# Optimization experiments

Hardware: AMD Instinct MI355X
Metric: run time of the kernel (lower is better)

The kernel has to match this reference:

```python
import jax, jax.numpy as jnp
import numpy as np

N_NODES = 50000
N_EDGES = 1600000
D_IN = 128
D_HID = 128
D_OUT = 128


def setup_inputs() -> dict:
    key = jax.random.key(0)
    k = jax.random.split(key, 6)
    feat = jax.random.normal(k[0], (N_NODES, D_IN), dtype=jnp.float32)
    W1 = jax.random.normal(k[1], (D_IN, D_HID), dtype=jnp.float32) * (1.0 / np.sqrt(D_IN))
    b1 = jnp.zeros((D_HID,), dtype=jnp.float32)
    W2 = jax.random.normal(k[2], (D_HID, D_OUT), dtype=jnp.float32) * (1.0 / np.sqrt(D_HID))
    b2 = jnp.zeros((D_OUT,), dtype=jnp.float32)
    src = jax.random.randint(k[3], (N_EDGES,), 0, N_NODES, dtype=jnp.int32)
    dst = jax.random.randint(k[4], (N_EDGES,), 0, N_NODES, dtype=jnp.int32)
    return {"feat": feat, "W1": W1, "b1": b1, "W2": W2, "b2": b2, "src": src, "dst": dst}


def _graph_conv(h, W, b, src, dst, norm_src, norm_dst, n_nodes):
    # DGL GraphConv, norm='both': h_src * out_deg^-1/2 -> sum over edges -> * in_deg^-1/2 -> W, +b
    h = h * norm_src[:, None]
    agg = jax.ops.segment_sum(h[src], dst, num_segments=n_nodes)
    agg = agg * norm_dst[:, None]
    return agg @ W + b


def reference(feat, W1, b1, W2, b2, src, dst):
    n = feat.shape[0]
    # dgl.add_self_loop: append (i, i) for every node
    loop = jnp.arange(n, dtype=src.dtype)
    src = jnp.concatenate([src, loop])
    dst = jnp.concatenate([dst, loop])
    ones = jnp.ones(src.shape[0], dtype=feat.dtype)
    out_deg = jax.ops.segment_sum(ones, src, num_segments=n)  # >= 1 due to self-loops
    in_deg = jax.ops.segment_sum(ones, dst, num_segments=n)
    norm_src = jax.lax.rsqrt(out_deg)
    norm_dst = jax.lax.rsqrt(in_deg)
    h = _graph_conv(feat, W1, b1, src, dst, norm_src, norm_dst, n)
    h = jax.nn.relu(h)
    h = _graph_conv(h, W2, b2, src, dst, norm_src, norm_dst, n)
    return h[None, :, :]  # unsqueeze(0) -> [1, N, out_features]
```

## Files before the change

### kernel.cpp

```cpp
#include <hip/hip_runtime.h>

#define D 128
#define RANGES 4
#define CHUNKS 64
#define BINS_MAX 12512

typedef unsigned short u16;


__device__ __forceinline__ u16 f2bf(float x) {
  unsigned u = __float_as_uint(x);
  u += 0x7fffu + ((u >> 16) & 1u);
  return (u16)(u >> 16);
}
#define BF_LO(u) __uint_as_float((u) << 16)
#define BF_HI(u) __uint_as_float((u) & 0xffff0000u)


__global__ __launch_bounds__(1024)
void hist_kernel(const int* __restrict__ keys, u16* __restrict__ part,
                 int E, int N, int binsR, int chunkE)
{
  __shared__ int hist[BINS_MAX];
  const int b = blockIdx.x;
  const int r = b & (RANGES - 1);
  const int k = b >> 2;
  const int lo = r * binsR;
  const int hi = min(N, lo + binsR);
  const int nb = hi - lo;
  for (int i = threadIdx.x; i < nb; i += 1024) hist[i] = 0;
  __syncthreads();
  const int e0 = k * chunkE;
  const int e1 = min(E, e0 + chunkE);
  for (int e = e0 + threadIdx.x; e < e1; e += 1024) {
    int v = keys[e];
    if (v >= lo && v < hi) atomicAdd(&hist[v - lo], 1);
  }
  __syncthreads();
  for (int i = threadIdx.x; i < nb; i += 1024)
    part[(size_t)k * N + lo + i] = (u16)hist[i];
}

__global__ void reduce_kernel(const u16* __restrict__ psrc, u16* __restrict__ pdst,
                              int* __restrict__ deg_in, float* __restrict__ nsrc,
                              float* __restrict__ ndst, int N)
{
  int bin = blockIdx.x * blockDim.x + threadIdx.x;
  if (bin >= N) return;
  int runs = 0, rund = 0;
  for (int k = 0; k < CHUNKS; ++k) {
    runs += psrc[(size_t)k * N + bin];
    int vd = pdst[(size_t)k * N + bin];
    pdst[(size_t)k * N + bin] = (u16)rund;
    rund += vd;
  }
  deg_in[bin] = rund;
  nsrc[bin] = rsqrtf((float)runs + 1.0f);
  ndst[bin] = rsqrtf((float)rund + 1.0f);
}


__global__ __launch_bounds__(1024)
void scan1_kernel(const int* __restrict__ din, int* __restrict__ roff,
                  int* __restrict__ bsum, int N)
{
  __shared__ int wsum[16];
  const int t = threadIdx.x, lane = t & 63, wid = t >> 6;
  const int i = blockIdx.x * 1024 + t;
  int v = (i < N) ? din[i] : 0;
  int x = v;
  #pragma unroll
  for (int off = 1; off < 64; off <<= 1) {
    int u = __shfl_up(x, off);
    if (lane >= off) x += u;
  }
  if (lane == 63) wsum[wid] = x;
  __syncthreads();
  if (wid == 0) {
    int y = (lane < 16) ? wsum[lane] : 0;
    int z = y;
    #pragma unroll
    for (int off = 1; off < 16; off <<= 1) {
      int u = __shfl_up(z, off);
      if (lane >= off) z += u;
    }
    if (lane < 16) wsum[lane] = z - y;
    if (lane == 15) bsum[blockIdx.x] = z;
  }
  __syncthreads();
  if (i < N) roff[i] = wsum[wid] + (x - v);
}

__global__ void scan2_kernel(int* __restrict__ bsum, int* __restrict__ roffN, int nb)
{
  const int t = threadIdx.x;
  int v = (t < nb) ? bsum[t] : 0;
  int x = v;
  #pragma unroll
  for (int off = 1; off < 64; off <<= 1) {
    int u = __shfl_up(x, off);
    if (t >= off) x += u;
  }
  if (t < nb) bsum[t] = x - v;
  if (t == 63) *roffN = x;
}

__global__ __launch_bounds__(1024)
void scan3_kernel(int* __restrict__ roff, const int* __restrict__ bsum, int N)
{
  const int i = blockIdx.x * 1024 + threadIdx.x;
  if (i < N) roff[i] += bsum[i >> 10];
}


__global__ __launch_bounds__(1024)
void scatter_kernel(const int* __restrict__ src, const int* __restrict__ dst,
                    const u16* __restrict__ pdst, const int* __restrict__ roff,
                    int* __restrict__ eout, int E, int N, int binsR, int chunkE)
{
  __shared__ int cur[BINS_MAX];
  const int b = blockIdx.x;
  const int r = b & (RANGES - 1);
  const int k = b >> 2;
  const int lo = r * binsR;
  const int hi = min(N, lo + binsR);
  const int nb = hi - lo;
  for (int i = threadIdx.x; i < nb; i += 1024)
    cur[i] = roff[lo + i] + (int)pdst[(size_t)k * N + lo + i];
  __syncthreads();
  const int e0 = k * chunkE;
  const int e1 = min(E, e0 + chunkE);
  for (int e = e0 + threadIdx.x; e < e1; e += 1024) {
    int d = dst[e];
    if (d >= lo && d < hi) eout[atomicAdd(&cur[d - lo], 1)] = src[e];
  }
}


__global__ __launch_bounds__(256)
void convert_kernel(const float* __restrict__ f, const float* __restrict__ nsrc,
                    unsigned* __restrict__ fb, int n4)
{
  const int i = blockIdx.x * blockDim.x + threadIdx.x;
  if (i < n4) {
    float s = nsrc[i >> 5];
    float4 v = ((const float4*)f)[i];
    uint2 o;
    o.x = (unsigned)f2bf(v.x * s) | ((unsigned)f2bf(v.y * s) << 16);
    o.y = (unsigned)f2bf(v.z * s) | ((unsigned)f2bf(v.w * s) << 16);
    ((uint2*)fb)[i] = o;
  }
}


__global__ __launch_bounds__(256)
void gather_bf_kernel(const unsigned* __restrict__ fb, const int* __restrict__ eidx,
                      const int* __restrict__ roff, const float* __restrict__ ndst,
                      float* __restrict__ out, int N)
{
  const int wid = threadIdx.x >> 6;
  const int lane = threadIdx.x & 63;
  const int node = blockIdx.x * 4 + wid;
  if (node >= N) return;
  const int h = lane >> 5;
  const int q = lane & 31;
  const uint2* fb2 = (const uint2*)fb;
  float4 acc = make_float4(0.f, 0.f, 0.f, 0.f);
  if (h == 0) {
    uint2 u = fb2[(size_t)node * 32 + q];
    acc.x = BF_LO(u.x); acc.y = BF_HI(u.x);
    acc.z = BF_LO(u.y); acc.w = BF_HI(u.y);
  }
  const int beg = roff[node], end = roff[node + 1];
  for (int e0 = beg; e0 < end; e0 += 64) {
    const int cnt = min(64, end - e0);
    int id = (lane < cnt) ? eidx[e0 + lane] : 0;
    int j = 0;
    for (; j + 16 <= cnt; j += 16) {
      int s0 = __shfl(id, j + 0 + h);
      int s1 = __shfl(id, j + 2 + h);
      int s2 = __shfl(id, j + 4 + h);
      int s3 = __shfl(id, j + 6 + h);
      int s4 = __shfl(id, j + 8 + h);
      int s5 = __shfl(id, j + 10 + h);
      int s6 = __shfl(id, j + 12 + h);
      int s7 = __shfl(id, j + 14 + h);
      uint2 u0 = fb2[(size_t)s0 * 32 + q];
      uint2 u1 = fb2[(size_t)s1 * 32 + q];
      uint2 u2 = fb2[(size_t)s2 * 32 + q];
      uint2 u3 = fb2[(size_t)s3 * 32 + q];
      uint2 u4 = fb2[(size_t)s4 * 32 + q];
      uint2 u5 = fb2[(size_t)s5 * 32 + q];
      uint2 u6 = fb2[(size_t)s6 * 32 + q];
      uint2 u7 = fb2[(size_t)s7 * 32 + q];
      acc.x += BF_LO(u0.x); acc.y += BF_HI(u0.x); acc.z += BF_LO(u0.y); acc.w += BF_HI(u0.y);
      acc.x += BF_LO(u1.x); acc.y += BF_HI(u1.x); acc.z += BF_LO(u1.y); acc.w += BF_HI(u1.y);
      acc.x += BF_LO(u2.x); acc.y += BF_HI(u2.x); acc.z += BF_LO(u2.y); acc.w += BF_HI(u2.y);
      acc.x += BF_LO(u3.x); acc.y += BF_HI(u3.x); acc.z += BF_LO(u3.y); acc.w += BF_HI(u3.y);
      acc.x += BF_LO(u4.x); acc.y += BF_HI(u4.x); acc.z += BF_LO(u4.y); acc.w += BF_HI(u4.y);
      acc.x += BF_LO(u5.x); acc.y += BF_HI(u5.x); acc.z += BF_LO(u5.y); acc.w += BF_HI(u5.y);
      acc.x += BF_LO(u6.x); acc.y += BF_HI(u6.x); acc.z += BF_LO(u6.y); acc.w += BF_HI(u6.y);
      acc.x += BF_LO(u7.x); acc.y += BF_HI(u7.x); acc.z += BF_LO(u7.y); acc.w += BF_HI(u7.y);
    }
    for (; j < cnt; j += 2) {
      int ej = j + h;
      int s = __shfl(id, ej & 63);
      if (ej < cnt) {
        uint2 u = fb2[(size_t)s * 32 + q];
        acc.x += BF_LO(u.x); acc.y += BF_HI(u.x);
        acc.z += BF_LO(u.y); acc.w += BF_HI(u.y);
      }
    }
  }
  acc.x += __shfl_xor(acc.x, 32);
  acc.y += __shfl_xor(acc.y, 32);
  acc.z += __shfl_xor(acc.z, 32);
  acc.w += __shfl_xor(acc.w, 32);
  if (h == 0) {
    float nd = ndst[node];
    acc.x *= nd; acc.y *= nd; acc.z *= nd; acc.w *= nd;
    *(float4*)(out + (size_t)node * D + q * 4) = acc;
  }
}


template<bool RELU_SCALE, bool BF_OUT>
__global__ __launch_bounds__(256)
void gemm128(const float* __restrict__ A, const float* __restrict__ W,
             const float* __restrict__ bias, const float* __restrict__ nsrc,
             void* __restrict__ Cv, int N)
{
  __shared__ float As[64][36];
  __shared__ float Bs[32][128];
  const int t = threadIdx.x;
  const int tx = t & 15;
  const int ty = t >> 4;
  const int r0 = blockIdx.x * 64;
  float acc[4][8];
  #pragma unroll
  for (int j = 0; j < 4; ++j)
    #pragma unroll
    for (int cc = 0; cc < 8; ++cc) acc[j][cc] = 0.f;

  for (int kc = 0; kc < D; kc += 32) {
    __syncthreads();
    #pragma unroll
    for (int m = 0; m < 2; ++m) {
      int q = t * 2 + m;
      int row = q >> 3;
      int fc = q & 7;
      int gr = r0 + row; if (gr > N - 1) gr = N - 1;
      float4 v = *(const float4*)(A + (size_t)gr * D + kc + fc * 4);
      *(float4*)(&As[row][fc * 4]) = v;
    }
    #pragma unroll
    for (int m = 0; m < 4; ++m) {
      int q = t + 256 * m;
      int kk = q >> 5;
      int fc = q & 31;
      float4 v = *(const float4*)(W + (size_t)(kc + kk) * D + fc * 4);
      *(float4*)(&Bs[kk][fc * 4]) = v;
    }
    __syncthreads();
    #pragma unroll
    for (int k = 0; k < 32; ++k) {
      float a0 = As[ty * 4 + 0][k];
      float a1 = As[ty * 4 + 1][k];
      float a2 = As[ty * 4 + 2][k];
      float a3 = As[ty * 4 + 3][k];
      float4 bv0 = *(const float4*)(&Bs[k][tx * 4]);
      float4 bv1 = *(const float4*)(&Bs[k][64 + tx * 4]);
      float bb[8] = {bv0.x, bv0.y, bv0.z, bv0.w, bv1.x, bv1.y, bv1.z, bv1.w};
      #pragma unroll
      for (int cc = 0; cc < 8; ++cc) {
        acc[0][cc] += a0 * bb[cc];
        acc[1][cc] += a1 * bb[cc];
        acc[2][cc] += a2 * bb[cc];
        acc[3][cc] += a3 * bb[cc];
      }
    }
  }

  float4 bb0 = *(const float4*)(bias + tx * 4);
  float4 bb1 = *(const float4*)(bias + 64 + tx * 4);
  float bb[8] = {bb0.x, bb0.y, bb0.z, bb0.w, bb1.x, bb1.y, bb1.z, bb1.w};
  #pragma unroll
  for (int j = 0; j < 4; ++j) {
    int gr = r0 + ty * 4 + j;
    if (gr < N) {
      float s = RELU_SCALE ? nsrc[gr] : 1.0f;
      float o[8];
      #pragma unroll
      for (int cc = 0; cc < 8; ++cc) {
        float v = acc[j][cc] + bb[cc];
        if (RELU_SCALE) v = fmaxf(v, 0.f) * s;
        o[cc] = v;
      }
      if (BF_OUT) {
        u16* Cb = (u16*)Cv;
        ushort4 w0, w1;
        w0.x = f2bf(o[0]); w0.y = f2bf(o[1]); w0.z = f2bf(o[2]); w0.w = f2bf(o[3]);
        w1.x = f2bf(o[4]); w1.y = f2bf(o[5]); w1.z = f2bf(o[6]); w1.w = f2bf(o[7]);
        *(ushort4*)(Cb + (size_t)gr * D + tx * 4) = w0;
        *(ushort4*)(Cb + (size_t)gr * D + 64 + tx * 4) = w1;
      } else {
        float* C = (float*)Cv;
        *(float4*)(C + (size_t)gr * D + tx * 4) = make_float4(o[0], o[1], o[2], o[3]);
        *(float4*)(C + (size_t)gr * D + 64 + tx * 4) = make_float4(o[4], o[5], o[6], o[7]);
      }
    }
  }
}


extern "C" void kernel_launch(void* const* d_in, const int* in_sizes, int n_in,
                              void* d_out, int out_size, void* d_ws, size_t ws_size,
                              hipStream_t stream) {
  const float* feat = (const float*)d_in[0];
  const float* W1   = (const float*)d_in[1];
  const float* b1   = (const float*)d_in[2];
  const float* W2   = (const float*)d_in[3];
  const float* b2   = (const float*)d_in[4];
  const int*   src  = (const int*)d_in[5];
  const int*   dst  = (const int*)d_in[6];
  const int N = in_sizes[0] / D;
  const int E = in_sizes[5];
  float* out = (float*)d_out;

  const int binsR = (N + RANGES - 1) / RANGES;
  const int chunkE = (((E + CHUNKS - 1) / CHUNKS) + 3) & ~3;

  auto align256 = [](size_t x) { return (x + 255) & ~(size_t)255; };
  char* p = (char*)d_ws;
  char* p0 = p;  p += align256((size_t)E * 4);
  char* p1 = p;  p += align256((size_t)N * D * 2);
  char* p2 = p;  p += align256((size_t)N * D * 2);
  int*   deg_in  = (int*)p;   p += align256((size_t)N * 4);
  int*   row_off = (int*)p;   p += align256((size_t)(N + 1) * 4);
  float* nsrc    = (float*)p; p += align256((size_t)N * 4);
  float* ndst    = (float*)p; p += align256((size_t)N * 4);
  int*   bsum    = (int*)p;   p += 256;

  u16*      psrc   = (u16*)p0;
  int*      esrc   = (int*)p0;
  u16*      pdst   = (u16*)p1;
  u16*      h1bf   = (u16*)p1;
  unsigned* featbf = (unsigned*)p2;

  const int nblk = (N + 1023) / 1024;

  hist_kernel<<<RANGES * CHUNKS, 1024, 0, stream>>>(src, psrc, E, N, binsR, chunkE);
  hist_kernel<<<RANGES * CHUNKS, 1024, 0, stream>>>(dst, pdst, E, N, binsR, chunkE);
  reduce_kernel<<<(N + 255) / 256, 256, 0, stream>>>(psrc, pdst, deg_in, nsrc, ndst, N);
  convert_kernel<<<(N * D / 4 + 255) / 256, 256, 0, stream>>>(feat, nsrc, featbf, N * D / 4);
  scan1_kernel<<<nblk, 1024, 0, stream>>>(deg_in, row_off, bsum, N);
  scan2_kernel<<<1, 64, 0, stream>>>(bsum, row_off + N, nblk);
  scan3_kernel<<<nblk, 1024, 0, stream>>>(row_off, bsum, N);
  scatter_kernel<<<RANGES * CHUNKS, 1024, 0, stream>>>(src, dst, pdst, row_off, esrc, E, N, binsR, chunkE);

  gather_bf_kernel<<<(N + 3) / 4, 256, 0, stream>>>(featbf, esrc, row_off, ndst, out, N);
  gemm128<true, true><<<(N + 63) / 64, 256, 0, stream>>>(out, W1, b1, nsrc, h1bf, N);
  gather_bf_kernel<<<(N + 3) / 4, 256, 0, stream>>>((const unsigned*)h1bf, esrc, row_off, ndst, out, N);
  gemm128<false, false><<<(N + 63) / 64, 256, 0, stream>>>(out, W2, b2, nsrc, out, N);
}
```

Baseline: 314.4 us.

## Store edge indices as u16 and aggregated features as bf16

Edge source indices are stored as 16-bit values, which halves CSR index traffic. The gather kernels write bf16 aggregates instead of fp32, and the GEMMs read and expand bf16 inputs, which halves the intermediate write and read volume. This is a risk: with N=50000 the indices fit in 16 bits only because N is below 65536, and it breaks for larger graphs. The extra bf16 rounding of the aggregates adds precision loss, and buffers are aliased into the output and workspace regions.

```diff
diff --git a/kernel.cpp b/kernel.cpp
--- a/kernel.cpp
+++ b/kernel.cpp
@@ -116,7 +116,7 @@
 __global__ __launch_bounds__(1024)
 void scatter_kernel(const int* __restrict__ src, const int* __restrict__ dst,
                     const u16* __restrict__ pdst, const int* __restrict__ roff,
-                    int* __restrict__ eout, int E, int N, int binsR, int chunkE)
+                    u16* __restrict__ eout, int E, int N, int binsR, int chunkE)
 {
   __shared__ int cur[BINS_MAX];
   const int b = blockIdx.x;
@@ -132,7 +132,7 @@
   const int e1 = min(E, e0 + chunkE);
   for (int e = e0 + threadIdx.x; e < e1; e += 1024) {
     int d = dst[e];
-    if (d >= lo && d < hi) eout[atomicAdd(&cur[d - lo], 1)] = src[e];
+    if (d >= lo && d < hi) eout[atomicAdd(&cur[d - lo], 1)] = (u16)src[e];
   }
 }
 
@@ -154,9 +154,9 @@
 
 
 __global__ __launch_bounds__(256)
-void gather_bf_kernel(const unsigned* __restrict__ fb, const int* __restrict__ eidx,
+void gather_bf_kernel(const unsigned* __restrict__ fb, const u16* __restrict__ eidx,
                       const int* __restrict__ roff, const float* __restrict__ ndst,
-                      float* __restrict__ out, int N)
+                      u16* __restrict__ outb, int N)
 {
   const int wid = threadIdx.x >> 6;
   const int lane = threadIdx.x & 63;
@@ -174,7 +174,7 @@
   const int beg = roff[node], end = roff[node + 1];
   for (int e0 = beg; e0 < end; e0 += 64) {
     const int cnt = min(64, end - e0);
-    int id = (lane < cnt) ? eidx[e0 + lane] : 0;
+    int id = (lane < cnt) ? (int)eidx[e0 + lane] : 0;
     int j = 0;
     for (; j + 16 <= cnt; j += 16) {
       int s0 = __shfl(id, j + 0 + h);
@@ -218,15 +218,17 @@
   acc.w += __shfl_xor(acc.w, 32);
   if (h == 0) {
     float nd = ndst[node];
-    acc.x *= nd; acc.y *= nd; acc.z *= nd; acc.w *= nd;
-    *(float4*)(out + (size_t)node * D + q * 4) = acc;
+    ushort4 w;
+    w.x = f2bf(acc.x * nd); w.y = f2bf(acc.y * nd);
+    w.z = f2bf(acc.z * nd); w.w = f2bf(acc.w * nd);
+    *(ushort4*)(outb + (size_t)node * D + q * 4) = w;
   }
 }
 
 
 template<bool RELU_SCALE, bool BF_OUT>
 __global__ __launch_bounds__(256)
-void gemm128(const float* __restrict__ A, const float* __restrict__ W,
+void gemm128(const u16* __restrict__ A, const float* __restrict__ W,
              const float* __restrict__ bias, const float* __restrict__ nsrc,
              void* __restrict__ Cv, int N)
 {
@@ -244,14 +246,16 @@
 
   for (int kc = 0; kc < D; kc += 32) {
     __syncthreads();
-    #pragma unroll
-    for (int m = 0; m < 2; ++m) {
-      int q = t * 2 + m;
-      int row = q >> 3;
-      int fc = q & 7;
+    {
+      int q2 = t * 2;
+      int row = q2 >> 3;
+      int fc = q2 & 7;
       int gr = r0 + row; if (gr > N - 1) gr = N - 1;
-      float4 v = *(const float4*)(A + (size_t)gr * D + kc + fc * 4);
-      *(float4*)(&As[row][fc * 4]) = v;
+      uint4 u = *(const uint4*)(A + (size_t)gr * D + kc + fc * 4);
+      float4 f0 = make_float4(BF_LO(u.x), BF_HI(u.x), BF_LO(u.y), BF_HI(u.y));
+      float4 f1 = make_float4(BF_LO(u.z), BF_HI(u.z), BF_LO(u.w), BF_HI(u.w));
+      *(float4*)(&As[row][fc * 4]) = f0;
+      *(float4*)(&As[row][fc * 4 + 4]) = f1;
     }
     #pragma unroll
     for (int m = 0; m < 4; ++m) {
@@ -332,7 +336,7 @@
 
   auto align256 = [](size_t x) { return (x + 255) & ~(size_t)255; };
   char* p = (char*)d_ws;
-  char* p0 = p;  p += align256((size_t)E * 4);
+  char* p0 = p;  p += align256((size_t)CHUNKS * N * 2);
   char* p1 = p;  p += align256((size_t)N * D * 2);
   char* p2 = p;  p += align256((size_t)N * D * 2);
   int*   deg_in  = (int*)p;   p += align256((size_t)N * 4);
@@ -342,10 +346,12 @@
   int*   bsum    = (int*)p;   p += 256;
 
   u16*      psrc   = (u16*)p0;
-  int*      esrc   = (int*)p0;
+  u16*      esrc   = (u16*)p0;
   u16*      pdst   = (u16*)p1;
   u16*      h1bf   = (u16*)p1;
   unsigned* featbf = (unsigned*)p2;
+  u16*      agg2   = (u16*)p2;
+  u16*      agg1   = (u16*)((char*)d_out + (size_t)N * D * 2);
 
   const int nblk = (N + 1023) / 1024;
 
@@ -358,8 +364,8 @@
   scan3_kernel<<<nblk, 1024, 0, stream>>>(row_off, bsum, N);
   scatter_kernel<<<RANGES * CHUNKS, 1024, 0, stream>>>(src, dst, pdst, row_off, esrc, E, N, binsR, chunkE);
 
-  gather_bf_kernel<<<(N + 3) / 4, 256, 0, stream>>>(featbf, esrc, row_off, ndst, out, N);
-  gemm128<true, true><<<(N + 63) / 64, 256, 0, stream>>>(out, W1, b1, nsrc, h1bf, N);
-  gather_bf_kernel<<<(N + 3) / 4, 256, 0, stream>>>((const unsigned*)h1bf, esrc, row_off, ndst, out, N);
-  gemm128<false, false><<<(N + 63) / 64, 256, 0, stream>>>(out, W2, b2, nsrc, out, N);
-}
+  gather_bf_kernel<<<(N + 3) / 4, 256, 0, stream>>>(featbf, esrc, row_off, ndst, agg1, N);
+  gemm128<true, true><<<(N + 63) / 64, 256, 0, stream>>>(agg1, W1, b1, nsrc, h1bf, N);
+  gather_bf_kernel<<<(N + 3) / 4, 256, 0, stream>>>((const unsigned*)h1bf, esrc, row_off, ndst, agg2, N);
+  gemm128<false, false><<<(N + 63) / 64, 256, 0, stream>>>(agg2, W2, b2, nsrc, out, N);
+}
```

After: 306.5 us. 1.03x faster.
